# Optimization experiments

Measured on AMD Instinct MI355X. Metric: run time of the kernel, lower is better.

Reference implementation:

```python
import jax, jax.numpy as jnp
import numpy as np
import math

D_K = 64

def setup_inputs() -> dict:
    key = jax.random.key(0)
    k1, k2, k3, k4 = jax.random.split(key, 4)
    B, H, S, D = 2, 16, 2048, D_K
    query = jax.random.normal(k1, (B, H, S, D), dtype=jnp.float32)
    kk = jax.random.normal(k2, (B, H, S, D), dtype=jnp.float32)
    value = jax.random.normal(k3, (B, H, S, D), dtype=jnp.float32)
    mask = jax.random.randint(k4, (B, 1, S, S), 0, 2).astype(bool)
    return {"query": query, "key": kk, "value": value, "mask": mask}

def reference(query, key, value, mask):
    # score = Q K^T / sqrt(d_k)  -> [B,H,S,S]
    score = jnp.einsum('bhqd,bhkd->bhqk', query, key) * (1.0 / math.sqrt(D_K))
    # masked_fill(mask, -inf)
    score = jnp.where(mask, -jnp.inf, score)
    attn = jax.nn.softmax(score, axis=-1)
    # rows that are fully masked produce NaN -> 0 (torch.nan_to_num)
    attn = jnp.nan_to_num(attn, nan=0.0)
    # dropout with drop_rate=0 is identity
    return jnp.einsum('bhqk,bhkd->bhqd', attn, value)
```

## Files before the change

### kernel.cpp

```cpp
#include <hip/hip_runtime.h>
#include <hip/hip_bf16.h>


#define S_LEN 2048
#define D_DIM 64
#define BH    32
#define BM    64
#define BN    64
#define NW    4
#define PST   72
#define QSCALE 0.1803368801f

typedef __bf16 bf16_t;
typedef bf16_t bf16x8 __attribute__((ext_vector_type(8)));
typedef float  f32x4  __attribute__((ext_vector_type(4)));
typedef unsigned short u16;
typedef unsigned char  u8;
typedef unsigned long long u64b;

__device__ __forceinline__ void load_lds16(const bf16_t* g, bf16_t* l) {
    __builtin_amdgcn_global_load_lds(
        (const __attribute__((address_space(1))) void*)g,
        (__attribute__((address_space(3))) void*)l, 16, 0, 0);
}

template<int CTRL>
__device__ __forceinline__ float dppmov(float v) {
    return __builtin_bit_cast(float,
        __builtin_amdgcn_update_dpp(0, __builtin_bit_cast(int, v),
                                    CTRL, 0xF, 0xF, true));
}
__device__ __forceinline__ float redsum16(float v) {
    v += dppmov<0xB1>(v);
    v += dppmov<0x4E>(v);
    v += dppmov<0x141>(v);
    v += dppmov<0x140>(v);
    return v;
}

__global__ __launch_bounds__(256)
void mask_to_bits(const unsigned* __restrict__ M, u64b* __restrict__ bm)
{
    const int t = threadIdx.x;
    unsigned p = M[(t * 8179) & ((1 << 21) - 1)];
    const int is_u8 = __syncthreads_or(p > 1u);
    const int id = blockIdx.x * 256 + t;
    u64b w = 0;
    if (is_u8) {
        const uint4* src = (const uint4*)((const u8*)M + (size_t)id * 64);
        #pragma unroll
        for (int g = 0; g < 4; ++g) {
            uint4 x = src[g];
            const unsigned dw[4] = {x.x, x.y, x.z, x.w};
            #pragma unroll
            for (int q = 0; q < 4; ++q) {
                const unsigned v = dw[q];
                const int base = g * 16 + q * 4;
                if (v & 0x000000FFu) w |= 1ull << (base + 0);
                if (v & 0x0000FF00u) w |= 1ull << (base + 1);
                if (v & 0x00FF0000u) w |= 1ull << (base + 2);
                if (v & 0xFF000000u) w |= 1ull << (base + 3);
            }
        }
    } else {
        const uint4* src = (const uint4*)(M + (size_t)id * 64);
        #pragma unroll
        for (int g = 0; g < 16; ++g) {
            uint4 x = src[g];
            if (x.x) w |= 1ull << (g * 4 + 0);
            if (x.y) w |= 1ull << (g * 4 + 1);
            if (x.z) w |= 1ull << (g * 4 + 2);
            if (x.w) w |= 1ull << (g * 4 + 3);
        }
    }
    bm[id] = w;
}

__global__ __launch_bounds__(256)
void qk_prep(const float* __restrict__ Q, const float* __restrict__ K,
             bf16_t* __restrict__ Qb, bf16_t* __restrict__ Kb)
{
    const size_t i = ((size_t)blockIdx.x * 256 + threadIdx.x) * 8;
    {
        float4 a = *(const float4*)(Q + i);
        float4 b = *(const float4*)(Q + i + 4);
        bf16x8 w;
        w[0]=(bf16_t)(a.x*QSCALE); w[1]=(bf16_t)(a.y*QSCALE);
        w[2]=(bf16_t)(a.z*QSCALE); w[3]=(bf16_t)(a.w*QSCALE);
        w[4]=(bf16_t)(b.x*QSCALE); w[5]=(bf16_t)(b.y*QSCALE);
        w[6]=(bf16_t)(b.z*QSCALE); w[7]=(bf16_t)(b.w*QSCALE);
        *(bf16x8*)(Qb + i) = w;
    }
    {
        float4 a = *(const float4*)(K + i);
        float4 b = *(const float4*)(K + i + 4);
        bf16x8 w;
        w[0]=(bf16_t)a.x; w[1]=(bf16_t)a.y; w[2]=(bf16_t)a.z; w[3]=(bf16_t)a.w;
        w[4]=(bf16_t)b.x; w[5]=(bf16_t)b.y; w[6]=(bf16_t)b.z; w[7]=(bf16_t)b.w;
        const size_t r = i >> 6;
        const int    g = (int)((i & 63) >> 3);
        *(bf16x8*)(Kb + r * 64 + ((g ^ (int)(r & 7)) * 8)) = w;
    }
}

__global__ __launch_bounds__(256)
void v_transpose(const float* __restrict__ V, bf16_t* __restrict__ Vt)
{
    __shared__ bf16_t T[128][PST];
    const int t  = threadIdx.x;
    const int sc = blockIdx.x;
    const int bh = blockIdx.y;
    const float* Vh = V + ((size_t)bh * S_LEN + sc * 128) * D_DIM;
    #pragma unroll
    for (int it = 0; it < 4; ++it) {
        const int row = it * 32 + (t >> 3);
        const int c8  = (t & 7) * 8;
        float4 a = *(const float4*)(Vh + row * D_DIM + c8);
        float4 b = *(const float4*)(Vh + row * D_DIM + c8 + 4);
        bf16_t* d = &T[row][c8];
        d[0]=(bf16_t)a.x; d[1]=(bf16_t)a.y; d[2]=(bf16_t)a.z; d[3]=(bf16_t)a.w;
        d[4]=(bf16_t)b.x; d[5]=(bf16_t)b.y; d[6]=(bf16_t)b.z; d[7]=(bf16_t)b.w;
    }
    __syncthreads();
    const int d = t >> 2;
    #pragma unroll
    for (int g = 0; g < 4; ++g) {
        const int s_off = (t & 3) * 32 + g * 8;
        const int kbt   = sc * 2 + (s_off >> 6);
        const int k_in  = s_off & 63;
        const int gk    = k_in >> 3;
        bf16x8 w;
        #pragma unroll
        for (int j = 0; j < 8; ++j) w[j] = T[s_off + j][d];
        *(bf16x8*)(Vt + (((size_t)bh * (S_LEN/BN) + kbt) * D_DIM + d) * 64
                      + ((gk ^ (d & 7)) * 8)) = w;
    }
}

__global__ __launch_bounds__(256, 3)
void fa_fwd(const float* __restrict__ Q, const float* __restrict__ K,
            const float* __restrict__ V, const void* __restrict__ M,
            const u64b* __restrict__ bm, const bf16_t* __restrict__ Qb,
            const bf16_t* __restrict__ Kb, const bf16_t* __restrict__ Vt,
            float* __restrict__ O)
{
    __shared__ __align__(16) bf16_t KldsA[BN * D_DIM];
    __shared__ __align__(16) bf16_t KldsB[BN * D_DIM];
    __shared__ __align__(16) bf16_t VldsA[D_DIM * BN];
    __shared__ __align__(16) bf16_t VldsB[D_DIM * BN];
    __shared__ __align__(16) bf16_t Plds[NW][16 * PST];

    const int tid  = threadIdx.x;
    const int wave = tid >> 6;
    const int lane = tid & 63;
    const int quad = lane >> 4;
    const int ln   = lane & 15;

    const int qt = blockIdx.x;
    const int bh = blockIdx.y;
    const int b  = bh >> 4;
    const int qbase = qt * BM + wave * 16;

    const size_t head_off = (size_t)bh * S_LEN * D_DIM;
    const float* Qh = Q + head_off;
    const float* Kh = K + head_off;
    const float* Vh = V + head_off;
    const bf16_t* Kbh = Kb ? (Kb + head_off) : nullptr;
    const u8*  Mb8  = (const u8*)M  + (size_t)b * S_LEN * S_LEN;
    const int* Mb32 = (const int*)M + (size_t)b * S_LEN * S_LEN;

    int mask_is_u8 = 0;
    if (!bm) {
        int probe = ((const int*)M)[(tid * 8179) & ((1 << 21) - 1)];
        mask_is_u8 = __syncthreads_or((unsigned)probe > 1u);
    }

    bf16x8 qfrag[2];
    if (Qb) {
        const bf16_t* qrow = Qb + head_off + (size_t)(qbase + ln) * D_DIM;
        qfrag[0] = *(const bf16x8*)(qrow + quad * 8);
        qfrag[1] = *(const bf16x8*)(qrow + 32 + quad * 8);
    } else {
        const float* qrow = Qh + (size_t)(qbase + ln) * D_DIM;
        #pragma unroll
        for (int s = 0; s < 2; ++s) {
            float4 a = *(const float4*)(qrow + s * 32 + quad * 8);
            float4 c = *(const float4*)(qrow + s * 32 + quad * 8 + 4);
            bf16x8 w;
            w[0]=(bf16_t)(a.x*QSCALE); w[1]=(bf16_t)(a.y*QSCALE);
            w[2]=(bf16_t)(a.z*QSCALE); w[3]=(bf16_t)(a.w*QSCALE);
            w[4]=(bf16_t)(c.x*QSCALE); w[5]=(bf16_t)(c.y*QSCALE);
            w[6]=(bf16_t)(c.z*QSCALE); w[7]=(bf16_t)(c.w*QSCALE);
            qfrag[s] = w;
        }
    }

    f32x4 accO[4] = {{0.f,0.f,0.f,0.f},{0.f,0.f,0.f,0.f},
                     {0.f,0.f,0.f,0.f},{0.f,0.f,0.f,0.f}};
    float lpart[4] = {0.f, 0.f, 0.f, 0.f};

    const size_t bmrow_base = ((size_t)b * S_LEN + qbase + quad * 4) * 32;
    const int xg = ln & 7;

    auto load_wm = [&](int kb, u64b* wm) {
        if (bm) {
            #pragma unroll
            for (int r = 0; r < 4; ++r)
                wm[r] = bm[bmrow_base + (size_t)r * 32 + (kb >> 6)];
        } else if (mask_is_u8) {
            #pragma unroll
            for (int r = 0; r < 4; ++r) {
                const u8* mp = Mb8 + (size_t)(qbase + quad*4 + r) * S_LEN + kb + ln;
                u64b w = 0;
                #pragma unroll
                for (int t = 0; t < 4; ++t)
                    if (mp[16*t]) w |= 1ull << (16*t + ln);
                wm[r] = w;
            }
        } else {
            #pragma unroll
            for (int r = 0; r < 4; ++r) {
                const int* mp = Mb32 + (size_t)(qbase + quad*4 + r) * S_LEN + kb + ln;
                u64b w = 0;
                #pragma unroll
                for (int t = 0; t < 4; ++t)
                    if (mp[16*t]) w |= 1ull << (16*t + ln);
                wm[r] = w;
            }
        }
    };

    auto prefetch = [&](int kb, bf16_t* Kl, bf16_t* Vl) {
        const bf16_t* kt = Kbh + (size_t)kb * D_DIM;
        const bf16_t* vt = Vt + ((size_t)bh * (S_LEN/BN) + (kb >> 6)) * (BN * D_DIM);
        #pragma unroll
        for (int i = 0; i < 2; ++i) {
            const int c = wave + 4 * i;
            load_lds16(kt + c * 512 + lane * 8, Kl + c * 512);
            load_lds16(vt + c * 512 + lane * 8, Vl + c * 512);
        }
    };

    auto compute_tile = [&](const bf16_t* Kl, const bf16_t* Vl, const u64b* wm) {
        f32x4 Sacc[4] = {{0.f,0.f,0.f,0.f},{0.f,0.f,0.f,0.f},
                         {0.f,0.f,0.f,0.f},{0.f,0.f,0.f,0.f}};
        #pragma unroll
        for (int s = 0; s < 2; ++s) {
            #pragma unroll
            for (int t = 0; t < 4; ++t) {
                bf16x8 bk = *(const bf16x8*)
                    &Kl[(16*t + ln) * D_DIM + (((s*4 + quad) ^ xg) * 8)];
                Sacc[t] = __builtin_amdgcn_mfma_f32_16x16x32_bf16(qfrag[s], bk, Sacc[t], 0, 0, 0);
            }
        }
        #pragma unroll
        for (int r = 0; r < 4; ++r) {
            const u64b wl = wm[r] >> ln;
            float ps[4];
            ps[0] = ( wl        & 1ull) ? 0.f : __builtin_amdgcn_exp2f(Sacc[0][r]);
            ps[1] = ((wl >> 16) & 1ull) ? 0.f : __builtin_amdgcn_exp2f(Sacc[1][r]);
            ps[2] = ((wl >> 32) & 1ull) ? 0.f : __builtin_amdgcn_exp2f(Sacc[2][r]);
            ps[3] = ((wl >> 48) & 1ull) ? 0.f : __builtin_amdgcn_exp2f(Sacc[3][r]);
            lpart[r] += (ps[0] + ps[1]) + (ps[2] + ps[3]);
            #pragma unroll
            for (int t = 0; t < 4; ++t)
                Plds[wave][(quad*4 + r) * PST + 16*t + ln] = (bf16_t)ps[t];
        }
        __asm__ volatile("" ::: "memory");
        #pragma unroll
        for (int s2 = 0; s2 < 2; ++s2) {
            bf16x8 pa = *(const bf16x8*)&Plds[wave][ln * PST + s2*32 + quad*8];
            #pragma unroll
            for (int dt = 0; dt < 4; ++dt) {
                bf16x8 bv = *(const bf16x8*)
                    &Vl[(16*dt + ln) * D_DIM + (((s2*4 + quad) ^ xg) * 8)];
                accO[dt] = __builtin_amdgcn_mfma_f32_16x16x32_bf16(pa, bv, accO[dt], 0, 0, 0);
            }
        }
    };

    if (Kbh) {
        prefetch(0, KldsA, VldsA);
        for (int kb = 0; kb < S_LEN; kb += 2 * BN) {
            u64b wm[4];
            __syncthreads();
            load_wm(kb, wm);
            if (kb + BN < S_LEN) prefetch(kb + BN, KldsB, VldsB);
            compute_tile(KldsA, VldsA, wm);
            __syncthreads();
            load_wm(kb + BN, wm);
            if (kb + 2*BN < S_LEN) prefetch(kb + 2*BN, KldsA, VldsA);
            compute_tile(KldsB, VldsB, wm);
        }
    } else {
        const int srow = tid >> 2;
        const int sgrp = tid & 3;
        for (int kb = 0; kb < S_LEN; kb += BN) {
            __syncthreads();
            const float* kp = Kh + (size_t)(kb + srow) * D_DIM + sgrp * 16;
            #pragma unroll
            for (int h = 0; h < 2; ++h) {
                float4 a = *(const float4*)(kp + h * 8);
                float4 c = *(const float4*)(kp + h * 8 + 4);
                bf16x8 w;
                w[0]=(bf16_t)a.x; w[1]=(bf16_t)a.y; w[2]=(bf16_t)a.z; w[3]=(bf16_t)a.w;
                w[4]=(bf16_t)c.x; w[5]=(bf16_t)c.y; w[6]=(bf16_t)c.z; w[7]=(bf16_t)c.w;
                const int g = sgrp * 2 + h;
                *(bf16x8*)&KldsA[srow * D_DIM + ((g ^ (srow & 7)) * 8)] = w;
            }
            const float* vp = Vh + (size_t)(kb + srow) * D_DIM + sgrp * 16;
            float vv[16];
            #pragma unroll
            for (int g = 0; g < 4; ++g) {
                float4 a = *(const float4*)(vp + g * 4);
                vv[g*4+0]=a.x; vv[g*4+1]=a.y; vv[g*4+2]=a.z; vv[g*4+3]=a.w;
            }
            const int gk = srow >> 3;
            #pragma unroll
            for (int jj = 0; jj < 16; ++jj) {
                const int j = (jj + srow) & 15;
                const int d = sgrp * 16 + j;
                VldsA[d * D_DIM + ((gk ^ (d & 7)) * 8) + (srow & 7)] = (bf16_t)vv[j];
            }
            __syncthreads();
            u64b wm[4];
            load_wm(kb, wm);
            compute_tile(KldsA, VldsA, wm);
        }
    }

    #pragma unroll
    for (int r = 0; r < 4; ++r) {
        const float l = redsum16(lpart[r]);
        const float inv = (l > 0.f) ? 1.f / l : 0.f;
        float* orow = O + head_off + (size_t)(qbase + quad*4 + r) * D_DIM;
        #pragma unroll
        for (int dt = 0; dt < 4; ++dt)
            orow[16*dt + ln] = accO[dt][r] * inv;
    }
}

extern "C" void kernel_launch(void* const* d_in, const int* in_sizes, int n_in,
                              void* d_out, int out_size, void* d_ws, size_t ws_size,
                              hipStream_t stream) {
    (void)in_sizes; (void)n_in; (void)out_size;
    const float* Q = (const float*)d_in[0];
    const float* K = (const float*)d_in[1];
    const float* V = (const float*)d_in[2];
    const void*  M = d_in[3];
    float* O = (float*)d_out;

    const size_t bm_bytes = (size_t)2 * S_LEN * (S_LEN / 64) * 8;
    const size_t kv_elems = (size_t)BH * S_LEN * D_DIM;
    const size_t need_all = bm_bytes + 3 * kv_elems * sizeof(bf16_t);

    u64b*   bm = (ws_size >= bm_bytes) ? (u64b*)d_ws : nullptr;
    bf16_t* Qb = nullptr; bf16_t* Kb = nullptr; bf16_t* Vt = nullptr;
    if (ws_size >= need_all) {
        Qb = (bf16_t*)((char*)d_ws + bm_bytes);
        Kb = Qb + kv_elems;
        Vt = Kb + kv_elems;
    }

    if (bm)
        mask_to_bits<<<dim3(131072 / 256), dim3(256), 0, stream>>>(
            (const unsigned*)M, bm);
    if (Kb) {
        qk_prep<<<dim3((unsigned)(kv_elems / 8 / 256)), dim3(256), 0, stream>>>(Q, K, Qb, Kb);
        v_transpose<<<dim3(S_LEN / 128, BH), dim3(256), 0, stream>>>(V, Vt);
    }

    dim3 grid(S_LEN / BM, BH);
    fa_fwd<<<grid, dim3(256), 0, stream>>>(Q, K, V, M, bm, Qb, Kb, Vt, O);
}
```

Baseline: 198.4 us.

## Compute transposed scores so P feeds PV MFMA from registers, drop P LDS round-trip

Swaps the MFMA operand order so each lane holds scores for one query row across contiguous keys. The probabilities can then be packed directly into f16 A-fragments for a 16x16x16 f16 MFMA, with no trip through shared memory. V is staged as f16 to match, and the separate Q bf16 prep kernel is dropped in favour of converting Q inside the kernel. It also raises launch_bounds occupancy to 4 and simplifies the row-sum reduction with shuffles. The cost is more, smaller MFMAs for the PV product, and f16 range limits on the P and V values.

New measurement: 181.0 us. 1.1x faster.

```diff
diff --git a/kernel.cpp b/kernel.cpp
--- a/kernel.cpp
+++ b/kernel.cpp
@@ -7,35 +7,21 @@
 #define BH    32
 #define BM    64
 #define BN    64
-#define NW    4
 #define PST   72
 #define QSCALE 0.1803368801f
 
-typedef __bf16 bf16_t;
+typedef __bf16    bf16_t;
+typedef _Float16  f16_t;
 typedef bf16_t bf16x8 __attribute__((ext_vector_type(8)));
+typedef f16_t  f16x4  __attribute__((ext_vector_type(4)));
 typedef float  f32x4  __attribute__((ext_vector_type(4)));
-typedef unsigned short u16;
 typedef unsigned char  u8;
 typedef unsigned long long u64b;
 
-__device__ __forceinline__ void load_lds16(const bf16_t* g, bf16_t* l) {
+__device__ __forceinline__ void load_lds16(const void* g, void* l) {
     __builtin_amdgcn_global_load_lds(
         (const __attribute__((address_space(1))) void*)g,
         (__attribute__((address_space(3))) void*)l, 16, 0, 0);
-}
-
-template<int CTRL>
-__device__ __forceinline__ float dppmov(float v) {
-    return __builtin_bit_cast(float,
-        __builtin_amdgcn_update_dpp(0, __builtin_bit_cast(int, v),
-                                    CTRL, 0xF, 0xF, true));
-}
-__device__ __forceinline__ float redsum16(float v) {
-    v += dppmov<0xB1>(v);
-    v += dppmov<0x4E>(v);
-    v += dppmov<0x141>(v);
-    v += dppmov<0x140>(v);
-    return v;
 }
 
 __global__ __launch_bounds__(256)
@@ -77,36 +63,23 @@
 }
 
 __global__ __launch_bounds__(256)
-void qk_prep(const float* __restrict__ Q, const float* __restrict__ K,
-             bf16_t* __restrict__ Qb, bf16_t* __restrict__ Kb)
+void k_prep(const float* __restrict__ K, bf16_t* __restrict__ Kb)
 {
     const size_t i = ((size_t)blockIdx.x * 256 + threadIdx.x) * 8;
-    {
-        float4 a = *(const float4*)(Q + i);
-        float4 b = *(const float4*)(Q + i + 4);
-        bf16x8 w;
-        w[0]=(bf16_t)(a.x*QSCALE); w[1]=(bf16_t)(a.y*QSCALE);
-        w[2]=(bf16_t)(a.z*QSCALE); w[3]=(bf16_t)(a.w*QSCALE);
-        w[4]=(bf16_t)(b.x*QSCALE); w[5]=(bf16_t)(b.y*QSCALE);
-        w[6]=(bf16_t)(b.z*QSCALE); w[7]=(bf16_t)(b.w*QSCALE);
-        *(bf16x8*)(Qb + i) = w;
-    }
-    {
-        float4 a = *(const float4*)(K + i);
-        float4 b = *(const float4*)(K + i + 4);
-        bf16x8 w;
-        w[0]=(bf16_t)a.x; w[1]=(bf16_t)a.y; w[2]=(bf16_t)a.z; w[3]=(bf16_t)a.w;
-        w[4]=(bf16_t)b.x; w[5]=(bf16_t)b.y; w[6]=(bf16_t)b.z; w[7]=(bf16_t)b.w;
-        const size_t r = i >> 6;
-        const int    g = (int)((i & 63) >> 3);
-        *(bf16x8*)(Kb + r * 64 + ((g ^ (int)(r & 7)) * 8)) = w;
-    }
+    float4 a = *(const float4*)(K + i);
+    float4 b = *(const float4*)(K + i + 4);
+    bf16x8 w;
+    w[0]=(bf16_t)a.x; w[1]=(bf16_t)a.y; w[2]=(bf16_t)a.z; w[3]=(bf16_t)a.w;
+    w[4]=(bf16_t)b.x; w[5]=(bf16_t)b.y; w[6]=(bf16_t)b.z; w[7]=(bf16_t)b.w;
+    const size_t r = i >> 6;
+    const int    g = (int)((i & 63) >> 3);
+    *(bf16x8*)(Kb + r * 64 + ((g ^ (int)(r & 7)) * 8)) = w;
 }
 
 __global__ __launch_bounds__(256)
-void v_transpose(const float* __restrict__ V, bf16_t* __restrict__ Vt)
+void v_transpose(const float* __restrict__ V, f16_t* __restrict__ Vt)
 {
-    __shared__ bf16_t T[128][PST];
+    __shared__ f16_t T[128][PST];
     const int t  = threadIdx.x;
     const int sc = blockIdx.x;
     const int bh = blockIdx.y;
@@ -117,9 +90,9 @@
         const int c8  = (t & 7) * 8;
         float4 a = *(const float4*)(Vh + row * D_DIM + c8);
         float4 b = *(const float4*)(Vh + row * D_DIM + c8 + 4);
-        bf16_t* d = &T[row][c8];
-        d[0]=(bf16_t)a.x; d[1]=(bf16_t)a.y; d[2]=(bf16_t)a.z; d[3]=(bf16_t)a.w;
-        d[4]=(bf16_t)b.x; d[5]=(bf16_t)b.y; d[6]=(bf16_t)b.z; d[7]=(bf16_t)b.w;
+        f16_t* d = &T[row][c8];
+        d[0]=(f16_t)a.x; d[1]=(f16_t)a.y; d[2]=(f16_t)a.z; d[3]=(f16_t)a.w;
+        d[4]=(f16_t)b.x; d[5]=(f16_t)b.y; d[6]=(f16_t)b.z; d[7]=(f16_t)b.w;
     }
     __syncthreads();
     const int d = t >> 2;
@@ -129,26 +102,26 @@
         const int kbt   = sc * 2 + (s_off >> 6);
         const int k_in  = s_off & 63;
         const int gk    = k_in >> 3;
-        bf16x8 w;
-        #pragma unroll
-        for (int j = 0; j < 8; ++j) w[j] = T[s_off + j][d];
-        *(bf16x8*)(Vt + (((size_t)bh * (S_LEN/BN) + kbt) * D_DIM + d) * 64
-                      + ((gk ^ (d & 7)) * 8)) = w;
-    }
-}
-
-__global__ __launch_bounds__(256, 3)
+        f16x4 w0, w1;
+        #pragma unroll
+        for (int j = 0; j < 4; ++j) { w0[j] = T[s_off + j][d]; w1[j] = T[s_off + 4 + j][d]; }
+        f16_t* dst = Vt + (((size_t)bh * (S_LEN/BN) + kbt) * D_DIM + d) * 64
+                        + ((gk ^ (d & 7)) * 8);
+        *(f16x4*)dst = w0;
+        *(f16x4*)(dst + 4) = w1;
+    }
+}
+
+__global__ __launch_bounds__(256, 4)
 void fa_fwd(const float* __restrict__ Q, const float* __restrict__ K,
             const float* __restrict__ V, const void* __restrict__ M,
-            const u64b* __restrict__ bm, const bf16_t* __restrict__ Qb,
-            const bf16_t* __restrict__ Kb, const bf16_t* __restrict__ Vt,
-            float* __restrict__ O)
+            const u64b* __restrict__ bm, const bf16_t* __restrict__ Kb,
+            const f16_t* __restrict__ Vt, float* __restrict__ O)
 {
     __shared__ __align__(16) bf16_t KldsA[BN * D_DIM];
     __shared__ __align__(16) bf16_t KldsB[BN * D_DIM];
-    __shared__ __align__(16) bf16_t VldsA[D_DIM * BN];
-    __shared__ __align__(16) bf16_t VldsB[D_DIM * BN];
-    __shared__ __align__(16) bf16_t Plds[NW][16 * PST];
+    __shared__ __align__(16) f16_t  VldsA[D_DIM * BN];
+    __shared__ __align__(16) f16_t  VldsB[D_DIM * BN];
 
     const int tid  = threadIdx.x;
     const int wave = tid >> 6;
@@ -176,11 +149,7 @@
     }
 
     bf16x8 qfrag[2];
-    if (Qb) {
-        const bf16_t* qrow = Qb + head_off + (size_t)(qbase + ln) * D_DIM;
-        qfrag[0] = *(const bf16x8*)(qrow + quad * 8);
-        qfrag[1] = *(const bf16x8*)(qrow + 32 + quad * 8);
-    } else {
+    {
         const float* qrow = Qh + (size_t)(qbase + ln) * D_DIM;
         #pragma unroll
         for (int s = 0; s < 2; ++s) {
@@ -197,42 +166,39 @@
 
     f32x4 accO[4] = {{0.f,0.f,0.f,0.f},{0.f,0.f,0.f,0.f},
                      {0.f,0.f,0.f,0.f},{0.f,0.f,0.f,0.f}};
-    float lpart[4] = {0.f, 0.f, 0.f, 0.f};
-
-    const size_t bmrow_base = ((size_t)b * S_LEN + qbase + quad * 4) * 32;
+    float lpart = 0.f;
+
     const int xg = ln & 7;
-
-    auto load_wm = [&](int kb, u64b* wm) {
-        if (bm) {
-            #pragma unroll
-            for (int r = 0; r < 4; ++r)
-                wm[r] = bm[bmrow_base + (size_t)r * 32 + (kb >> 6)];
-        } else if (mask_is_u8) {
-            #pragma unroll
-            for (int r = 0; r < 4; ++r) {
-                const u8* mp = Mb8 + (size_t)(qbase + quad*4 + r) * S_LEN + kb + ln;
-                u64b w = 0;
+    const size_t bmrow = ((size_t)b * S_LEN + qbase + ln) * 32;
+
+    auto load_wm = [&](int kb) -> u64b {
+        if (bm) return bm[bmrow + (kb >> 6)];
+        u64b w = 0;
+        if (mask_is_u8) {
+            const u8* mp = Mb8 + (size_t)(qbase + ln) * S_LEN + kb;
+            #pragma unroll
+            for (int t = 0; t < 4; ++t)
                 #pragma unroll
-                for (int t = 0; t < 4; ++t)
-                    if (mp[16*t]) w |= 1ull << (16*t + ln);
-                wm[r] = w;
-            }
+                for (int j = 0; j < 4; ++j) {
+                    const int k = t*16 + quad*4 + j;
+                    if (mp[k]) w |= 1ull << k;
+                }
         } else {
-            #pragma unroll
-            for (int r = 0; r < 4; ++r) {
-                const int* mp = Mb32 + (size_t)(qbase + quad*4 + r) * S_LEN + kb + ln;
-                u64b w = 0;
+            const int* mp = Mb32 + (size_t)(qbase + ln) * S_LEN + kb;
+            #pragma unroll
+            for (int t = 0; t < 4; ++t)
                 #pragma unroll
-                for (int t = 0; t < 4; ++t)
-                    if (mp[16*t]) w |= 1ull << (16*t + ln);
-                wm[r] = w;
-            }
-        }
+                for (int j = 0; j < 4; ++j) {
+                    const int k = t*16 + quad*4 + j;
+                    if (mp[k]) w |= 1ull << k;
+                }
+        }
+        return w;
     };
 
-    auto prefetch = [&](int kb, bf16_t* Kl, bf16_t* Vl) {
+    auto prefetch = [&](int kb, bf16_t* Kl, f16_t* Vl) {
         const bf16_t* kt = Kbh + (size_t)kb * D_DIM;
-        const bf16_t* vt = Vt + ((size_t)bh * (S_LEN/BN) + (kb >> 6)) * (BN * D_DIM);
+        const f16_t*  vt = Vt + ((size_t)bh * (S_LEN/BN) + (kb >> 6)) * (BN * D_DIM);
         #pragma unroll
         for (int i = 0; i < 2; ++i) {
             const int c = wave + 4 * i;
@@ -241,40 +207,38 @@
         }
     };
 
-    auto compute_tile = [&](const bf16_t* Kl, const bf16_t* Vl, const u64b* wm) {
-        f32x4 Sacc[4] = {{0.f,0.f,0.f,0.f},{0.f,0.f,0.f,0.f},
-                         {0.f,0.f,0.f,0.f},{0.f,0.f,0.f,0.f}};
+    auto compute_tile = [&](const bf16_t* Kl, const f16_t* Vl, u64b wm) {
+        f32x4 St[4] = {{0.f,0.f,0.f,0.f},{0.f,0.f,0.f,0.f},
+                       {0.f,0.f,0.f,0.f},{0.f,0.f,0.f,0.f}};
         #pragma unroll
         for (int s = 0; s < 2; ++s) {
             #pragma unroll
             for (int t = 0; t < 4; ++t) {
-                bf16x8 bk = *(const bf16x8*)
+                bf16x8 ak = *(const bf16x8*)
                     &Kl[(16*t + ln) * D_DIM + (((s*4 + quad) ^ xg) * 8)];
-                Sacc[t] = __builtin_amdgcn_mfma_f32_16x16x32_bf16(qfrag[s], bk, Sacc[t], 0, 0, 0);
-            }
-        }
-        #pragma unroll
-        for (int r = 0; r < 4; ++r) {
-            const u64b wl = wm[r] >> ln;
-            float ps[4];
-            ps[0] = ( wl        & 1ull) ? 0.f : __builtin_amdgcn_exp2f(Sacc[0][r]);
-            ps[1] = ((wl >> 16) & 1ull) ? 0.f : __builtin_amdgcn_exp2f(Sacc[1][r]);
-            ps[2] = ((wl >> 32) & 1ull) ? 0.f : __builtin_amdgcn_exp2f(Sacc[2][r]);
-            ps[3] = ((wl >> 48) & 1ull) ? 0.f : __builtin_amdgcn_exp2f(Sacc[3][r]);
-            lpart[r] += (ps[0] + ps[1]) + (ps[2] + ps[3]);
-            #pragma unroll
-            for (int t = 0; t < 4; ++t)
-                Plds[wave][(quad*4 + r) * PST + 16*t + ln] = (bf16_t)ps[t];
-        }
-        __asm__ volatile("" ::: "memory");
-        #pragma unroll
-        for (int s2 = 0; s2 < 2; ++s2) {
-            bf16x8 pa = *(const bf16x8*)&Plds[wave][ln * PST + s2*32 + quad*8];
+                St[t] = __builtin_amdgcn_mfma_f32_16x16x32_bf16(ak, qfrag[s], St[t], 0, 0, 0);
+            }
+        }
+        f16x4 pa[4];
+        #pragma unroll
+        for (int t = 0; t < 4; ++t) {
+            const unsigned nib = (unsigned)(wm >> (t*16 + quad*4)) & 0xFu;
+            #pragma unroll
+            for (int j = 0; j < 4; ++j) {
+                const float p = (nib & (1u << j)) ? 0.f
+                              : __builtin_amdgcn_exp2f(St[t][j]);
+                lpart += p;
+                pa[t][j] = (f16_t)p;
+            }
+        }
+        #pragma unroll
+        for (int t = 0; t < 4; ++t) {
             #pragma unroll
             for (int dt = 0; dt < 4; ++dt) {
-                bf16x8 bv = *(const bf16x8*)
-                    &Vl[(16*dt + ln) * D_DIM + (((s2*4 + quad) ^ xg) * 8)];
-                accO[dt] = __builtin_amdgcn_mfma_f32_16x16x32_bf16(pa, bv, accO[dt], 0, 0, 0);
+                const int g = 2*t + (quad >> 1);
+                f16x4 bv = *(const f16x4*)
+                    &Vl[(dt*16 + ln) * D_DIM + ((g ^ xg) * 8) + (quad & 1) * 4];
+                accO[dt] = __builtin_amdgcn_mfma_f32_16x16x16f16(pa[t], bv, accO[dt], 0, 0, 0);
             }
         }
     };
@@ -282,13 +246,12 @@
     if (Kbh) {
         prefetch(0, KldsA, VldsA);
         for (int kb = 0; kb < S_LEN; kb += 2 * BN) {
-            u64b wm[4];
             __syncthreads();
-            load_wm(kb, wm);
+            u64b wm = load_wm(kb);
             if (kb + BN < S_LEN) prefetch(kb + BN, KldsB, VldsB);
             compute_tile(KldsA, VldsA, wm);
             __syncthreads();
-            load_wm(kb + BN, wm);
+            wm = load_wm(kb + BN);
             if (kb + 2*BN < S_LEN) prefetch(kb + 2*BN, KldsA, VldsA);
             compute_tile(KldsB, VldsB, wm);
         }
@@ -320,19 +283,19 @@
             for (int jj = 0; jj < 16; ++jj) {
                 const int j = (jj + srow) & 15;
                 const int d = sgrp * 16 + j;
-                VldsA[d * D_DIM + ((gk ^ (d & 7)) * 8) + (srow & 7)] = (bf16_t)vv[j];
+                VldsA[d * D_DIM + ((gk ^ (d & 7)) * 8) + (srow & 7)] = (f16_t)vv[j];
             }
             __syncthreads();
-            u64b wm[4];
-            load_wm(kb, wm);
-            compute_tile(KldsA, VldsA, wm);
-        }
-    }
-
+            compute_tile(KldsA, VldsA, load_wm(kb));
+        }
+    }
+
+    lpart += __shfl_xor(lpart, 16, 64);
+    lpart += __shfl_xor(lpart, 32, 64);
     #pragma unroll
     for (int r = 0; r < 4; ++r) {
-        const float l = redsum16(lpart[r]);
-        const float inv = (l > 0.f) ? 1.f / l : 0.f;
+        const float lr  = __shfl(lpart, quad * 4 + r, 64);
+        const float inv = (lr > 0.f) ? 1.f / lr : 0.f;
         float* orow = O + head_off + (size_t)(qbase + quad*4 + r) * D_DIM;
         #pragma unroll
         for (int dt = 0; dt < 4; ++dt)
@@ -352,24 +315,23 @@
 
     const size_t bm_bytes = (size_t)2 * S_LEN * (S_LEN / 64) * 8;
     const size_t kv_elems = (size_t)BH * S_LEN * D_DIM;
-    const size_t need_all = bm_bytes + 3 * kv_elems * sizeof(bf16_t);
+    const size_t need_all = bm_bytes + 2 * kv_elems * 2;
 
     u64b*   bm = (ws_size >= bm_bytes) ? (u64b*)d_ws : nullptr;
-    bf16_t* Qb = nullptr; bf16_t* Kb = nullptr; bf16_t* Vt = nullptr;
+    bf16_t* Kb = nullptr; f16_t* Vt = nullptr;
     if (ws_size >= need_all) {
-        Qb = (bf16_t*)((char*)d_ws + bm_bytes);
-        Kb = Qb + kv_elems;
-        Vt = Kb + kv_elems;
+        Kb = (bf16_t*)((char*)d_ws + bm_bytes);
+        Vt = (f16_t*)(Kb + kv_elems);
     }
 
     if (bm)
         mask_to_bits<<<dim3(131072 / 256), dim3(256), 0, stream>>>(
             (const unsigned*)M, bm);
     if (Kb) {
-        qk_prep<<<dim3((unsigned)(kv_elems / 8 / 256)), dim3(256), 0, stream>>>(Q, K, Qb, Kb);
+        k_prep<<<dim3((unsigned)(kv_elems / 8 / 256)), dim3(256), 0, stream>>>(K, Kb);
         v_transpose<<<dim3(S_LEN / 128, BH), dim3(256), 0, stream>>>(V, Vt);
     }
 
     dim3 grid(S_LEN / BM, BH);
-    fa_fwd<<<grid, dim3(256), 0, stream>>>(Q, K, V, M, bm, Qb, Kb, Vt, O);
-}
+    fa_fwd<<<grid, dim3(256), 0, stream>>>(Q, K, V, M, bm, Kb, Vt, O);
+}
```
